# Kernel optimization log

Measured on AMD Instinct MI355X. Metric: run time of the kernel, lower is better.

Reference implementation:

```python
import jax, jax.numpy as jnp
import numpy as np

B, D, RES, NS, MAXS, ITERS = 64, 512, 16, 8, 64, 3
N = RES * RES            # ntokens
HID = max(D, 128)        # mlp hidden = max(dim, hidden_dim)
EPS = 1e-8
BETA = 0.99
SCALE = D ** -0.5


def _grid(res):
    rs = [np.linspace(0.0, 1.0, num=r) for r in (res, res)]
    g = np.stack(np.meshgrid(*rs, sparse=False, indexing='ij'), axis=-1)
    g = g.reshape(res, res, 2)[None].astype(np.float32)
    return jnp.asarray(np.concatenate([g, 1.0 - g], axis=-1))  # (1,res,res,4)


def _ln(x, g, b, axes):
    m = jnp.mean(x, axes, keepdims=True)
    v = jnp.var(x, axes, keepdims=True)
    return (x - m) * jax.lax.rsqrt(v + 1e-5) * g + b


def _gru(x, h, wih, whh, bih, bhh):
    gi = x @ wih.T + bih
    gh = h @ whh.T + bhh
    ir, iz, inn = jnp.split(gi, 3, -1)
    hr, hz, hn = jnp.split(gh, 3, -1)
    r = jax.nn.sigmoid(ir + hr)
    z = jax.nn.sigmoid(iz + hz)
    n = jnp.tanh(inn + r * hn)
    return (1.0 - z) * n + z * h


def setup_inputs() -> dict:
    key = jax.random.key(0)
    ks = iter(jax.random.split(key, 40))
    W = lambda *s: jax.random.normal(next(ks), s, jnp.float32) * 0.02
    Z = lambda *s: jnp.zeros(s, jnp.float32)
    O = lambda *s: jnp.ones(s, jnp.float32)
    inp = dict(
        x=jax.random.normal(next(ks), (B, D, RES, RES), jnp.float32),
        enc_pos_w=W(4, D), enc_pos_b=Z(D),
        enc_norm_g=O(N, D), enc_norm_b=Z(N, D),
        enc_mlp_w1=W(D, D), enc_mlp_b1=Z(D), enc_mlp_w2=W(D, D), enc_mlp_b2=Z(D),
        anch_w1=W(N, N), anch_b1=Z(N), anch_w2=W(N, N), anch_b2=Z(N),
        wq=W(D, D), bq=Z(D), wk=W(D, D), bk=Z(D), wv=W(D, D), bv=Z(D),
        gru_wih=W(3 * D, D), gru_whh=W(3 * D, D), gru_bih=Z(3 * D), gru_bhh=Z(3 * D),
        mlp_w1=W(D, HID), mlp_b1=Z(HID), mlp_w2=W(HID, D), mlp_b2=Z(D),
        ni_g=O(D), ni_b=Z(D), ns_g=O(D), ns_b=Z(D), npf_g=O(D), npf_b=Z(D),
        emb=jax.random.uniform(next(ks), (MAXS, D), jnp.float32, -1.0 / MAXS, 1.0 / MAXS),
        dec_pos_w=W(4, D), dec_pos_b=Z(D),
    )
    return inp


def reference(x, enc_pos_w, enc_pos_b, enc_norm_g, enc_norm_b,
              enc_mlp_w1, enc_mlp_b1, enc_mlp_w2, enc_mlp_b2,
              anch_w1, anch_b1, anch_w2, anch_b2,
              wq, bq, wk, bk, wv, bv,
              gru_wih, gru_whh, gru_bih, gru_bhh,
              mlp_w1, mlp_b1, mlp_w2, mlp_b2,
              ni_g, ni_b, ns_g, ns_b, npf_g, npf_b,
              emb, dec_pos_w, dec_pos_b):
    sg = jax.lax.stop_gradient
    grid = _grid(RES)
    f = jnp.transpose(x, (0, 2, 3, 1))                       # (B,RES,RES,D)
    # encoder_transformation(position=False): flatten + LayerNorm([N,D]) over last 2 dims
    f_np = _ln(f.reshape(B, N, D), enc_norm_g, enc_norm_b, (-2, -1))
    k_nopos = f_np @ wk + bk
    # encoder_transformation(position=True): +pos, LN([N,D]), feature MLP, then norm_input
    pos = grid @ enc_pos_w + enc_pos_b
    fp = _ln((f + pos).reshape(B, N, D), enc_norm_g, enc_norm_b, (-2, -1))
    fp = jax.nn.relu(fp @ enc_mlp_w1 + enc_mlp_b1) @ enc_mlp_w2 + enc_mlp_b2
    fp = _ln(fp, ni_g, ni_b, -1)
    k = fp @ wk + bk
    v = fp @ wv + bv
    # passthrough_eigen_basis on detached k_nopos: normalize, covariance, eigh
    xn = k_nopos / jnp.clip(jnp.linalg.norm(k_nopos, axis=-1, keepdims=True), 1e-12)
    cov = sg(jnp.einsum('bkf,bgf->bkg', xn, xn))             # (B,N,N)
    _, evec = jnp.linalg.eigh(cov)                           # ascending, like symeig
    eig_vec = jnp.transpose(evec[:, :, 1:NS + 1], (0, 2, 1))  # (B,NS,N)
    eig_vec = jax.nn.relu(eig_vec @ anch_w1 + anch_b1) @ anch_w2 + anch_b2
    z = jnp.einsum('bnf,bkn->bkf', f_np, eig_vec)            # masked_projection -> (B,NS,D)
    # sample_slotemb_traditional (euclidean, non-unique, update=0)
    zf = z.reshape(-1, D)
    tslots = emb @ wq + bq                                   # (MAXS,D)
    d2 = (zf ** 2).sum(1, keepdims=True) + (tslots ** 2).sum(1) - 2.0 * zf @ tslots.T
    sampled_dist = d2.min(1)
    idx = jnp.argmin(d2, 1)                                  # (B*NS,)
    # faithful reproduction of the original's index reordering (incl. its cross-batch quirk)
    order = jnp.argsort(sampled_dist.reshape(B, NS), axis=1).reshape(-1)
    idx = idx[order]
    z_q = emb[idx].reshape(B, NS, D)
    t_zq = tslots[idx].reshape(B, NS, D)
    qloss = ((sg(t_zq) - z) ** 2).sum() / B + BETA * ((t_zq - sg(z)) ** 2).sum() / B
    slots = z + sg(z_q - z)                                  # straight-through
    # slot attention iterations
    for _ in range(ITERS):
        slots_prev = slots
        q = _ln(slots, ns_g, ns_b, -1) @ wq + bq
        dots = jnp.einsum('bid,bjd->bij', q, k) * SCALE      # (B,NS,N)
        attn = jax.nn.softmax(dots, axis=1) + EPS            # competition over slots
        attn = attn / attn.sum(-1, keepdims=True)
        updates = jnp.einsum('bjd,bij->bid', v, attn)
        slots = _gru(updates.reshape(-1, D), slots_prev.reshape(-1, D),
                     gru_wih, gru_whh, gru_bih, gru_bhh).reshape(B, NS, D)
        h = _ln(slots, npf_g, npf_b, -1)
        slots = slots + (jax.nn.relu(h @ mlp_w1 + mlp_b1) @ mlp_w2 + mlp_b2)
    # decoder_transformation: broadcast slots over decoder grid + position embed
    dpos = grid @ dec_pos_w + dec_pos_b                      # (1,RES,RES,D)
    df = jnp.broadcast_to(slots.reshape(B * NS, 1, 1, D), (B * NS, RES, RES, D)) + dpos
    feats = jnp.transpose(df, (0, 3, 1, 2))                  # (B*NS,D,RES,RES)
    return feats, slots, idx.reshape(B, NS), qloss
```

## Files before the change

### kernel.cpp

```cpp
#include <hip/hip_runtime.h>
#include <math.h>
#include <stdint.h>


#define NB 64
#define ND 512
#define NN_ 256
#define NSL 8
#define LPB 24

static __device__ __forceinline__ double fsign(double a, double b) {
  return (b >= 0.0) ? fabs(a) : -fabs(a);
}
static __device__ __forceinline__ double dlapy2d(double x, double y) {
  double ax = fabs(x), ay = fabs(y);
  double w = ax > ay ? ax : ay, z = ax > ay ? ay : ax;
  if (z == 0.0) return w;
  double q = z / w;
  return w * sqrt(1.0 + q * q);
}
#define EPS_D 1.1102230246251565e-16

static __device__ void dlartgd(double f, double g, double& cs, double& sn, double& r) {
  if (g == 0.0) { cs = 1.0; sn = 0.0; r = f; }
  else if (f == 0.0) { cs = 0.0; sn = fsign(1.0, g); r = fabs(g); }
  else {
    double f1 = fabs(f);
    double d = sqrt(f * f + g * g);
    cs = f1 / d;
    r = fsign(d, f);
    sn = g / r;
  }
}

static __device__ void dlaev2d(double a, double b, double c, double& rt1, double& rt2,
                               double& cs1, double& sn1) {
  double sm = a + c, df = a - c, adf = fabs(df), tb = b + b, ab = fabs(tb);
  double acmx, acmn;
  if (fabs(a) > fabs(c)) { acmx = a; acmn = c; } else { acmx = c; acmn = a; }
  double rt;
  if (adf > ab) { double q = ab / adf; rt = adf * sqrt(1.0 + q * q); }
  else if (adf < ab) { double q = adf / ab; rt = ab * sqrt(1.0 + q * q); }
  else rt = ab * sqrt(2.0);
  int sgn1;
  if (sm < 0.0) { rt1 = 0.5 * (sm - rt); sgn1 = -1; rt2 = (acmx / rt1) * acmn - (b / rt1) * b; }
  else if (sm > 0.0) { rt1 = 0.5 * (sm + rt); sgn1 = 1; rt2 = (acmx / rt1) * acmn - (b / rt1) * b; }
  else { rt1 = 0.5 * rt; rt2 = -0.5 * rt; sgn1 = 1; }
  double cs; int sgn2;
  if (df >= 0.0) { cs = df + rt; sgn2 = 1; } else { cs = df - rt; sgn2 = -1; }
  double acs = fabs(cs);
  if (acs > ab) { double ct = -tb / cs; sn1 = 1.0 / sqrt(1.0 + ct * ct); cs1 = ct * sn1; }
  else {
    if (ab == 0.0) { cs1 = 1.0; sn1 = 0.0; }
    else { double tn = -cs / tb; cs1 = 1.0 / sqrt(1.0 + tn * tn); sn1 = tn * cs1; }
  }
  if (sgn1 == sgn2) { double tn = cs1; cs1 = -sn1; sn1 = tn; }
}

static __device__ void dsteqr16_lds(double* dd, double* ee, double* zz, int sw) {
  const int n = 16;
#define ZM(i, j) zz[((((i)-1) << 4) + ((j)-1)) ^ sw]
#define D_(i) dd[(i)]
// ... 356 lines not shown
  __syncthreads();
  for (int o = 128; o > 0; o >>= 1) { if (t < o) { s1[t] += s1[t + o]; s2[t] += s2[t + o]; } __syncthreads(); }
  double m = s1[0] / 512.0, var = s2[0] / 512.0 - m * m;
  float rstd = 1.0f / sqrtf((float)var + 1e-5f);
  float mf = (float)m;
  out[(size_t)r * 512 + t] = (v0 - mf) * rstd * g[t] + be[t];
  out[(size_t)r * 512 + t + 256] = (v1 - mf) * rstd * g[t + 256] + be[t + 256];
}

__global__ __launch_bounds__(256) void xnorm_kernel(float* kno) {
  int r = blockIdx.x, t = threadIdx.x;
  __shared__ double s1[256];
  float* row = kno + (size_t)r * 512;
  float v0 = row[t], v1 = row[t + 256];
  s1[t] = (double)v0 * v0 + (double)v1 * v1;
  __syncthreads();
  for (int o = 128; o > 0; o >>= 1) { if (t < o) s1[t] += s1[t + o]; __syncthreads(); }
  float nrm = fmaxf((float)sqrt(s1[0]), 1e-12f);
  row[t] = v0 / nrm; row[t + 256] = v1 / nrm;
}

__global__ __launch_bounds__(256) void cov_kernel(const float* __restrict__ xn, double* __restrict__ cov) {
  int b = blockIdx.x, it = blockIdx.y, jt = blockIdx.z;
  __shared__ float Xi[64][65], Xj[64][65];
  int t = threadIdx.x;
  int tx = t & 15, ty = t >> 4;
  double acc[4][4] = {};
  const float* xb = xn + (size_t)b * 131072;
  for (int f0 = 0; f0 < 512; f0 += 64) {
    for (int l = 0; l < 16; ++l) {
      int idx = t + l * 256;
      int r = idx >> 6, ff = idx & 63;
      Xi[r][ff] = xb[(size_t)(it * 64 + r) * 512 + f0 + ff];
      Xj[r][ff] = xb[(size_t)(jt * 64 + r) * 512 + f0 + ff];
    }
    __syncthreads();
    for (int ff = 0; ff < 64; ++ff) {
      double a0[4], b0[4];
#pragma unroll
      for (int q = 0; q < 4; ++q) { a0[q] = (double)Xi[ty * 4 + q][ff]; b0[q] = (double)Xj[tx * 4 + q][ff]; }
#pragma unroll
      for (int q = 0; q < 4; ++q)
#pragma unroll
        for (int p = 0; p < 4; ++p) acc[q][p] += a0[q] * b0[p];
    }
    __syncthreads();
  }
  double* cb = cov + (size_t)b * 65536;
  for (int q = 0; q < 4; ++q)
    for (int p = 0; p < 4; ++p)
      cb[(size_t)(it * 64 + ty * 4 + q) * 256 + jt * 64 + tx * 4 + p] = acc[q][p];
}

__global__ __launch_bounds__(1024) void dsytrd_kernel(double* Aall, double* dE, double* eE, double* tauE) {
  int b = blockIdx.x, t = threadIdx.x;
  int lane = t & 63, wid = t >> 6;
  double* A = Aall + (size_t)b * 65536;
  __shared__ double v[256], w[256];
  __shared__ double redw[16];
  const int n = 256;
  for (int i = 0; i < n - 1; ++i) {
    double s = 0.0;
    for (int r = i + 2 + t; r < n; r += 1024) { double xv = A[(size_t)r * 256 + i]; s += xv * xv; }
    for (int o = 1; o < 64; o <<= 1) s += __shfl_xor(s, o);
    if (lane == 0) redw[wid] = s;
    __syncthreads();
    double xns = 0.0;
    for (int k = 0; k < 16; ++k) xns += redw[k];
    double alpha = A[(size_t)(i + 1) * 256 + i];
    double tau, beta, scl;
    if (xns == 0.0) { tau = 0.0; beta = alpha; scl = 0.0; }
    else {
      double xnorm = sqrt(xns);
      double rr = dlapy2d(alpha, xnorm);
      beta = (alpha >= 0.0) ? -rr : rr;
      tau = (beta - alpha) / beta;
      scl = 1.0 / (alpha - beta);
    }
    if (tau != 0.0) {
      for (int r = i + 1 + t; r < n; r += 1024) {
        double vr = (r == i + 1) ? 1.0 : A[(size_t)r * 256 + i] * scl;
        v[r] = vr;
        if (r >= i + 2) A[(size_t)r * 256 + i] = vr;
      }
      __syncthreads();
      for (int r = i + 1 + wid; r < n; r += 16) {
        const double* Ar = A + (size_t)r * 256;
        double acc = 0.0;
        for (int c = i + 1 + lane; c < n; c += 64) acc += Ar[c] * v[c];
        for (int o = 1; o < 64; o <<= 1) acc += __shfl_xor(acc, o);
        if (lane == 0) w[r] = tau * acc;
      }
      __syncthreads();
      double sd = 0.0;
      for (int r = i + 1 + t; r < n; r += 1024) sd += w[r] * v[r];
      for (int o = 1; o < 64; o <<= 1) sd += __shfl_xor(sd, o);
      if (lane == 0) redw[wid] = sd;
      __syncthreads();
      double dot = 0.0;
      for (int k = 0; k < 16; ++k) dot += redw[k];
      double alpha2 = -0.5 * tau * dot;
      for (int r = i + 1 + t; r < n; r += 1024) w[r] += alpha2 * v[r];
      __syncthreads();
      for (int r = i + 1 + wid; r < n; r += 16) {
        double vr = v[r], wr = w[r];
        double* Ar = A + (size_t)r * 256;
        for (int c = i + 1 + lane; c < n; c += 64) Ar[c] -= vr * w[c] + wr * v[c];
      }
    }
    if (t == 0) { eE[b * 256 + i] = beta; tauE[b * 256 + i] = tau; }
    __syncthreads();
  }
  for (int r = t; r < n; r += 1024) dE[b * 256 + r] = A[(size_t)r * 256 + r];
}

__global__ __launch_bounds__(64) void tear_kernel(double* dE, const double* eE) {
  int b = threadIdx.x;
  if (b >= 64) return;
  for (int m = 1; m < 16; ++m) {
    int p = m * 16 - 1;
    double ae = fabs(eE[b * 256 + p]);
    dE[b * 256 + p] -= ae;
    dE[b * 256 + p + 1] -= ae;
  }
}

__global__ __launch_bounds__(64) void leaf_kernel(double* dE, double* eE, double* Qe, int* indxq) {
  __shared__ double Zs[LPB * 256];
  __shared__ double des[LPB * 33];
  int t = threadIdx.x;
  int g = blockIdx.x * LPB + t;
  if (t >= LPB || g >= 1024) return;
  int b = g >> 4, lf = g & 15, off = lf * 16;
  double* zz = Zs + t * 256;
  double* dd = des + t * 33;
  double* ee = dd + 16;
  int sw = t & 15;
  for (int i = 1; i <= 16; ++i) dd[i] = dE[b * 256 + off + i - 1];
  for (int i = 1; i <= 15; ++i) ee[i] = eE[b * 256 + off + i - 1];
  ee[16] = 0.0;
  dsteqr16_lds(dd, ee, zz, sw);
  for (int i = 1; i <= 16; ++i) dE[b * 256 + off + i - 1] = dd[i];
  double* Qb = Qe + (size_t)b * 65536;
  for (int r = 0; r < 16; ++r)
    for (int c = 0; c < 16; ++c) Qb[(size_t)(off + r) * 256 + off + c] = zz[((r << 4) + c) ^ sw];
  for (int i = 0; i < 16; ++i) indxq[b * 256 + off + i] = i + 1;
}

__global__ __launch_bounds__(64) void merge_scan_kernel(int nm, int nmerge, double* Qsrc, double* dE,
                                                        const double* eE, int* indxq, double* dlamda_g,
                                                        double* w_g, double* rho_g, int* surv_g,
                                                        int* defl_g, int* Kb) {
  int gid = blockIdx.x * 64 + threadIdx.x;
  if (gid >= 64 * nmerge) return;
  int b = gid / nmerge, mg = gid % nmerge;
  int off = mg * nm, n1 = nm / 2, n2 = nm - n1;
  double* Q = Qsrc + (size_t)b * 65536;
  double* dg = dE + b * 256 + off;
  int* iqg = indxq + b * 256 + off;

  double dl[257], zl[257], dlamA[257], wl2[257];
  int iq[257], indxc[257], indxl[257], indxpl[257];

  for (int i = 1; i <= nm; ++i) { dl[i] = dg[i - 1]; iq[i] = iqg[i - 1]; }
  double rho = eE[b * 256 + off + n1 - 1];
  for (int j = 1; j <= n1; ++j) zl[j] = Q[(size_t)(off + n1 - 1) * 256 + off + j - 1];
  for (int j = 1; j <= n2; ++j) zl[n1 + j] = Q[(size_t)(off + n1) * 256 + off + n1 + j - 1];
  if (rho < 0.0)
    for (int j = n1 + 1; j <= nm; ++j) zl[j] = -zl[j];
  double tconst = 1.0 / sqrt(2.0);
  for (int j = 1; j <= nm; ++j) zl[j] *= tconst;
  rho = fabs(2.0 * rho);
  rho_g[b * nmerge + mg] = rho;
  for (int i = n1 + 1; i <= nm; ++i) iq[i] += n1;
  for (int i = 1; i <= nm; ++i) dlamA[i] = dl[iq[i]];
  dlamrg_dev(n1, n2, dlamA, 1, 1, indxc);
  for (int i = 1; i <= nm; ++i) indxl[i] = iq[indxc[i]];
  int imax = 1, jmax = 1;
  for (int i = 2; i <= nm; ++i) {
    if (fabs(zl[i]) > fabs(zl[imax])) imax = i;
    if (fabs(dl[i]) > fabs(dl[jmax])) jmax = i;
  }
  double tol = 8.0 * EPS_D * fmax(fabs(dl[jmax]), fabs(zl[imax]));
  if (rho * fabs(zl[imax]) <= tol) {
    Kb[b * nmerge + mg] = 0;
    for (int j = 1; j <= nm; ++j) { defl_g[b * 256 + off + j - 1] = indxl[j]; dlamA[j] = dl[indxl[j]]; }
    for (int j = 1; j <= nm; ++j) { dg[j - 1] = dlamA[j]; iqg[j - 1] = j; }
    return;
  }
  int K = 0, K2 = nm + 1, pj = 0, j = 1;
  bool havepj = false;
  for (j = 1; j <= nm; ++j) {
    int nj = indxl[j];
    if (rho * fabs(zl[nj]) <= tol) {
      K2--; indxpl[K2] = nj;
      if (j == nm) break;
    } else { pj = nj; havepj = true; break; }
  }
  if (havepj) {
    for (;;) {
      j = j + 1;
      if (j > nm) break;
      int nj = indxl[j];
      if (rho * fabs(zl[nj]) <= tol) { K2--; indxpl[K2] = nj; }
      else {
        double s_ = zl[pj], c_ = zl[nj];
        double tau_ = dlapy2d(c_, s_);
        double t_ = dl[nj] - dl[pj];
        c_ = c_ / tau_; s_ = -s_ / tau_;
        if (fabs(t_ * c_ * s_) <= tol) {
          zl[nj] = tau_; zl[pj] = 0.0;
          int cp = off + pj - 1, cn = off + nj - 1;
          for (int r = 0; r < nm; ++r) {
            size_t rowb = (size_t)(off + r) * 256;
            double x = Q[rowb + cp], y = Q[rowb + cn];
            Q[rowb + cp] = c_ * x + s_ * y;
            Q[rowb + cn] = c_ * y - s_ * x;
          }
          double t2 = dl[pj] * c_ * c_ + dl[nj] * s_ * s_;
          dl[nj] = dl[pj] * s_ * s_ + dl[nj] * c_ * c_;
          dl[pj] = t2;
          K2--;
          int i_ = 1;
          for (;;) {
            if (K2 + i_ <= nm) {
              if (dl[pj] < dl[indxpl[K2 + i_]]) {
                indxpl[K2 + i_ - 1] = indxpl[K2 + i_];
                indxpl[K2 + i_] = pj;
                i_++;
              } else { indxpl[K2 + i_ - 1] = pj; break; }
            } else { indxpl[K2 + i_ - 1] = pj; break; }
          }
          pj = nj;
        } else {
          K++; dlamA[K] = dl[pj]; wl2[K] = zl[pj]; indxpl[K] = pj; pj = nj;
        }
      }
    }
    K++; dlamA[K] = dl[pj]; wl2[K] = zl[pj]; indxpl[K] = pj;
  }
  Kb[b * nmerge + mg] = K;
  for (int i = 1; i <= K; ++i) {
    dlamda_g[b * 256 + off + i - 1] = dlamA[i];
    w_g[b * 256 + off + i - 1] = wl2[i];
    surv_g[b * 256 + off + i - 1] = indxpl[i];
  }
  for (int jj = K + 1; jj <= nm; ++jj) {
    defl_g[b * 256 + off + jj - 1] = indxpl[jj];
    dg[jj - 1] = dl[indxpl[jj]];
  }
}

__global__ __launch_bounds__(256) void secular_kernel(int nm, int nmerge, const double* dlamda_g,
                                                      const double* w_g, const double* rho_g,
                                                      const int* Kb, double* dE, double* tau_g,
                                                      int* orig_g) {
  int b = blockIdx.x, pos = threadIdx.x;
  int mg = pos / nm, jl = pos % nm + 1;
  int K = Kb[b * nmerge + mg];
  if (jl > K) return;
  int base = b * 256 + mg * nm;
  const double* dl = dlamda_g + base;
  const double* w = w_g + base;
  double rho = rho_g[b * nmerge + mg];
  int orig; double lo, hi;
  if (jl < K) {
    double dj = dl[jl - 1], dj1 = dl[jl];
    double mid = (dj + dj1) * 0.5;
    double acc = 0.0;
    for (int i = 0; i < K; ++i) acc += w[i] * w[i] / (dl[i] - mid);
    double fmid = 1.0 + rho * acc;
    if (fmid > 0.0) { orig = jl; lo = 0.0; hi = mid - dj; }
    else { orig = jl + 1; lo = mid - dj1; hi = 0.0; }
  } else {
    orig = K;
    double zs = 0.0;
    for (int i = 0; i < K; ++i) zs += w[i] * w[i];
    lo = 0.0; hi = rho * zs;
  }
  double dorig = dl[orig - 1];
  for (int it = 0; it < 100; ++it) {
    double tm = 0.5 * (lo + hi);
    if (tm == lo || tm == hi) break;
    double acc = 0.0;
    for (int i = 0; i < K; ++i) acc += w[i] * w[i] / ((dl[i] - dorig) - tm);
    double g = 1.0 + rho * acc;
    if (g > 0.0) hi = tm; else lo = tm;
  }
  double tau = 0.5 * (lo + hi);
  tau_g[base + jl - 1] = tau;
  orig_g[base + jl - 1] = orig;
  dE[base + jl - 1] = dorig + tau;
}

__global__ __launch_bounds__(256) void zhat_kernel(int nm, int nmerge, const double* dlamda_g,
                                                   const double* w_g, const double* tau_g,
                                                   const int* orig_g, const int* Kb, double* zhat_g) {
  int b = blockIdx.x, pos = threadIdx.x;
  int mg = pos / nm, il = pos % nm + 1;
  int K = Kb[b * nmerge + mg];
  if (il > K) return;
  int base = b * 256 + mg * nm;
// ... 51 lines not shown
    if (dg[ind1 - 1] <= dg[ind2 - 1]) { idx[i++] = ind1; ind1++; n1sv--; }
    else { idx[i++] = ind2; ind2--; n2sv--; }
  }
  if (n1sv == 0) { while (n2sv > 0) { idx[i++] = ind2; ind2--; n2sv--; } }
  else { while (n1sv > 0) { idx[i++] = ind1; ind1++; n1sv--; } }
  for (int t = 1; t <= nm; ++t) iqg[t - 1] = idx[t];
}

__global__ __launch_bounds__(256) void merge_gemm_kernel(int nm, int nmerge, const double* Qsrc,
                                                         const double* Cbuf, const int* surv_g,
                                                         const int* Kb, double* Qdst) {
  int b = blockIdx.x, mg = blockIdx.y;
  int tcnt = nm / 32;
  int rt = blockIdx.z / tcnt, ct = blockIdx.z % tcnt;
  int off = mg * nm;
  int K = Kb[b * nmerge + mg];
  if (ct * 32 >= K) return;
  __shared__ double Qs[32][33];
  __shared__ double Cs[32][33];
  __shared__ int svs[32];
  int t = threadIdx.x;
  int tc = t & 31, tr = t >> 5;
  const double* Qsb = Qsrc + (size_t)b * 65536;
  const double* Cb = Cbuf + (size_t)b * 65536;
  double acc[4] = {0, 0, 0, 0};
  int r0 = off + rt * 32, c0 = off + ct * 32;
  for (int i0 = 0; i0 < K; i0 += 32) {
    if (t < 32) svs[t] = (i0 + t < K) ? surv_g[b * 256 + off + i0 + t] : 0;
    __syncthreads();
    for (int l = 0; l < 4; ++l) {
      int idx = t + l * 256;
      int r = idx >> 5, ii = idx & 31;
      int sc = svs[ii];
      Qs[r][ii] = (sc > 0) ? Qsb[(size_t)(r0 + r) * 256 + off + sc - 1] : 0.0;
      Cs[r][ii] = (i0 + r < K && ct * 32 + ii < K) ? Cb[(size_t)(off + i0 + r) * 256 + c0 + ii] : 0.0;
    }
    __syncthreads();
    for (int ii = 0; ii < 32; ++ii) {
      double cv = Cs[ii][tc];
#pragma unroll
      for (int q = 0; q < 4; ++q) acc[q] += Qs[tr * 4 + q][ii] * cv;
    }
    __syncthreads();
  }
  if (ct * 32 + tc < K) {
    double* Qd = Qdst + (size_t)b * 65536;
    for (int q = 0; q < 4; ++q) Qd[(size_t)(r0 + tr * 4 + q) * 256 + c0 + tc] = acc[q];
  }
}

__global__ __launch_bounds__(256) void defl_copy_kernel(int nm, int nmerge, const double* Qsrc,
                                                        const int* defl_g, const int* Kb,
                                                        double* Qdst) {
  int b = blockIdx.x, pos = threadIdx.x;
  int mg = pos / nm, jl = pos % nm + 1;
  int K = Kb[b * nmerge + mg];
  if (jl <= K) return;
  int off = mg * nm;
  int srcc = off + defl_g[b * 256 + off + jl - 1] - 1;
  int dstc = off + jl - 1;
  const double* Qs = Qsrc + (size_t)b * 65536;
  double* Qd = Qdst + (size_t)b * 65536;
  for (int r = 0; r < nm; ++r) Qd[(size_t)(off + r) * 256 + dstc] = Qs[(size_t)(off + r) * 256 + srcc];
}

__global__ __launch_bounds__(256) void dormtr_kernel(const double* Aall, const double* tauE,
                                                     const double* Qe, const int* indxq, float* E) {
  int b = blockIdx.x, t = threadIdx.x;
  const double* A = Aall + (size_t)b * 65536;
  __shared__ double U[256][8];
  __shared__ double wred[32][8];
  __shared__ double wfin[8];
  __shared__ int sel[8];
  if (t < 8) sel[t] = indxq[b * 256 + 1 + t] - 1;
  __syncthreads();
  for (int i = t; i < 256 * 8; i += 256) {
    int r = i >> 3, c = i & 7;
    U[r][c] = Qe[(size_t)b * 65536 + (size_t)r * 256 + sel[c]];
  }
  __syncthreads();
  int lane = t & 31, col = t >> 5;
  for (int s = 254; s >= 0; --s) {
    double tv = tauE[b * 256 + s];
    if (tv == 0.0) continue;
    double acc = (lane == 0) ? U[s + 1][col] : 0.0;
    for (int r = s + 2 + lane; r < 256; r += 32) acc += A[(size_t)r * 256 + s] * U[r][col];
    wred[lane][col] = acc;
    __syncthreads();
    if (t < 8) { double a = 0.0; for (int l2 = 0; l2 < 32; ++l2) a += wred[l2][t]; wfin[t] = a; }
    __syncthreads();
    double wc = wfin[col] * tv;
    if (lane == 0) U[s + 1][col] -= wc;
    for (int r = s + 2 + lane; r < 256; r += 32) U[r][col] -= A[(size_t)r * 256 + s] * wc;
    __syncthreads();
  }
  for (int i = t; i < 8 * 256; i += 256) {
    int s = i >> 8, nn = i & 255;
    E[((size_t)b * 8 + s) * 256 + nn] = (float)U[nn][s];
  }
}

__global__ __launch_bounds__(256) void zproj_kernel(const float* __restrict__ fnp,
                                                    const float* __restrict__ E2,
                                                    float* __restrict__ z) {
  int b = blockIdx.x, s = blockIdx.y;
  __shared__ float er[256];
  int t = threadIdx.x;
  er[t] = E2[((size_t)b * 8 + s) * 256 + t];
  __syncthreads();
  for (int d = t; d < 512; d += 256) {
    float acc = 0.f;
    for (int n = 0; n < 256; ++n) acc += er[n] * fnp[((size_t)b * 256 + n) * 512 + d];
    z[((size_t)b * 8 + s) * 512 + d] = acc;
  }
}

__global__ __launch_bounds__(64) void d2_kernel(const float* __restrict__ z,
                                                const float* __restrict__ ts, double* sdist,
                                                int* idxr) {
  int row = blockIdx.x;
  int lane = threadIdx.x;
  const float* zr = z + (size_t)row * 512;
  const float* tr = ts + (size_t)lane * 512;
  double zz = 0, zt = 0, tt = 0;
  for (int d = 0; d < 512; ++d) {
    double zv = zr[d], tv = tr[d];
    zz += zv * zv; zt += zv * tv; tt += tv * tv;
  }
  double d2 = zz + tt - 2.0 * zt;
  int best = lane; double bv = d2;
  for (int off = 32; off > 0; off >>= 1) {
    double ov = __shfl_down(bv, off);
    int oi = __shfl_down(best, off);
    if (ov < bv || (ov == bv && oi < best)) { bv = ov; best = oi; }
  }
  if (lane == 0) { sdist[row] = bv; idxr[row] = best; }
}

__global__ __launch_bounds__(64) void order_kernel(const double* sdist, const int* idxr, int* fidx,
                                                   float* out_idx) {
  int b = threadIdx.x;
  if (b >= 64) return;
  double sd[8]; int ord[8];
  for (int s = 0; s < 8; ++s) { sd[s] = sdist[b * 8 + s]; ord[s] = s; }
  for (int a = 1; a < 8; ++a) {
    double kv = sd[a]; int ko = ord[a]; int c = a - 1;
    while (c >= 0 && sd[c] > kv) { sd[c + 1] = sd[c]; ord[c + 1] = ord[c]; --c; }
    sd[c + 1] = kv; ord[c + 1] = ko;
  }
  for (int s = 0; s < 8; ++s) {
    int fi = idxr[ord[s]];
    fidx[b * 8 + s] = fi;
    out_idx[b * 8 + s] = (float)fi;
  }
}

__global__ __launch_bounds__(256) void slots0_kernel(const float* z, const float* emb,
                                                     const int* fidx, float* slots) {
  int i = blockIdx.x * 256 + threadIdx.x;
  if (i >= 512 * 512) return;
  int t = i / 512, d = i % 512;
  float zv = z[i];
  float zq = emb[fidx[t] * 512 + d];
  slots[i] = zv + (zq - zv);
}

// ... 183 lines not shown
  int* defl_g = (int*)alloc(64 * 256 * 4);
  int* orig_g = (int*)alloc(64 * 256 * 4);
  int* Kb = (int*)alloc(64 * 8 * 4);
  int* fidx = (int*)alloc(512 * 4);
  float* E = (float*)alloc(64 * 8 * 256 * 4);
  float* Eh = (float*)alloc(64 * 8 * 256 * 4);
  float* E2 = (float*)alloc(64 * 8 * 256 * 4);
  float* z = (float*)alloc(512 * 512 * 4);
  float* tslots = (float*)alloc(64 * 512 * 4);
  double* sdist = (double*)alloc(512 * 8);
  int* idxr = (int*)alloc(512 * 4);
  float* sA = (float*)alloc(512 * 512 * 4);
  float* sB = (float*)alloc(512 * 512 * 4);
  float* lnbuf = (float*)alloc(512 * 512 * 4);
  float* qbuf = (float*)alloc(512 * 512 * 4);
  float* dotsb = (float*)alloc(64 * 8 * 256 * 4);
  float* attnb = (float*)alloc(64 * 8 * 256 * 4);
  float* asumb = (float*)alloc(64 * 8 * 4);
  float* updb = (float*)alloc(512 * 512 * 4);
  float* gib = (float*)alloc((size_t)512 * 1536 * 4);
  float* ghb = (float*)alloc((size_t)512 * 1536 * 4);
  float* hidb = (float*)alloc(512 * 512 * 4);
  (void)ws_size; (void)in_sizes; (void)n_in; (void)out_size;

  auto gemm = [&](const float* A, const float* Bm, const float* bias, const float* base, float* C,
                  int M, int Nc, int Kd, int bt, int act, int addb) {
    if ((M % 128) == 0 && (Nc % 128) == 0 && (Kd % 16) == 0) {
      dim3 g(M / 128, Nc / 128);
      gemm_f32_big<<<g, 256, 0, stream>>>(A, Bm, bias, base, C, M, Nc, Kd, bt, act, addb);
    } else {
      dim3 g((M + 63) / 64, (Nc + 63) / 64);
      gemm_f32<<<g, 256, 0, stream>>>(A, Bm, bias, base, C, M, Nc, Kd, bt, act, addb);
    }
  };

  pos_kernel<<<(131072 + 255) / 256, 256, 0, stream>>>(enc_pos_w, enc_pos_b, posT);
  pos_kernel<<<(131072 + 255) / 256, 256, 0, stream>>>(dec_pos_w, dec_pos_b, dposT);
  stats_kernel<<<64, 256, 0, stream>>>(x, posT, m1, r1, 0);
  stats_kernel<<<64, 256, 0, stream>>>(x, posT, m2, r2, 1);
  tln_kernel<<<dim3(64, 16, 8), 256, 0, stream>>>(x, posT, enc_norm_g, enc_norm_b, m1, r1, m2, r2,
                                                  fnp, R3);
  gemm(fnp, wk, bk, nullptr, R2, 16384, 512, 512, 0, 0, 0);
  gemm(R3, enc_mlp_w1, enc_mlp_b1, nullptr, R4, 16384, 512, 512, 0, 1, 0);
  gemm(R4, enc_mlp_w2, enc_mlp_b2, nullptr, R5, 16384, 512, 512, 0, 0, 0);
  rowln_kernel<<<16384, 256, 0, stream>>>(R5, ni_g, ni_b, R5);
  gemm(R5, wk, bk, nullptr, kbuf, 16384, 512, 512, 0, 0, 0);
  gemm(R5, wv, bv, nullptr, vbuf, 16384, 512, 512, 0, 0, 0);
  xnorm_kernel<<<16384, 256, 0, stream>>>(R2);
  double* covA = (double*)R3;
  cov_kernel<<<dim3(64, 4, 4), 256, 0, stream>>>(R2, covA);
  double* Qe = (double*)R4;
  double* Q2 = (double*)R5;
  double* Cbuf = (double*)R2;
  hipMemsetAsync(Qe, 0, S, stream);
  hipMemsetAsync(Q2, 0, S, stream);
  dsytrd_kernel<<<64, 1024, 0, stream>>>(covA, dE, eE, tauE);
  tear_kernel<<<1, 64, 0, stream>>>(dE, eE);
  leaf_kernel<<<(1024 + LPB - 1) / LPB, LPB, 0, stream>>>(dE, eE, Qe, indxq);
  for (int L = 0; L < 4; ++L) {
    int nm = 32 << L;
    int nmerge = 256 / nm;
    double* src = (L % 2 == 0) ? Qe : Q2;
    double* dst = (L % 2 == 0) ? Q2 : Qe;
    int gScan = (64 * nmerge + 63) / 64;
    merge_scan_kernel<<<gScan, 64, 0, stream>>>(nm, nmerge, src, dE, eE, indxq, dlamda_g, w_g, rho_g,
                                                surv_g, defl_g, Kb);
    secular_kernel<<<64, 256, 0, stream>>>(nm, nmerge, dlamda_g, w_g, rho_g, Kb, dE, tau_g, orig_g);
    zhat_kernel<<<64, 256, 0, stream>>>(nm, nmerge, dlamda_g, w_g, tau_g, orig_g, Kb, zhat_g);
    coeff_kernel<<<64, 256, 0, stream>>>(nm, nmerge, dlamda_g, zhat_g, tau_g, orig_g, Kb, Cbuf);
    int tcnt = nm / 32;
    merge_gemm_kernel<<<dim3(64, nmerge, tcnt * tcnt), 256, 0, stream>>>(nm, nmerge, src, Cbuf,
                                                                         surv_g, Kb, dst);
    defl_copy_kernel<<<64, 256, 0, stream>>>(nm, nmerge, src, defl_g, Kb, dst);
    dlamrg_kernel<<<gScan, 64, 0, stream>>>(nm, nmerge, dE, Kb, indxq);
  }
  dormtr_kernel<<<64, 256, 0, stream>>>(covA, tauE, Qe, indxq, E);
  gemm(E, anch_w1, anch_b1, nullptr, Eh, 512, 256, 256, 0, 1, 0);
  gemm(Eh, anch_w2, anch_b2, nullptr, E2, 512, 256, 256, 0, 0, 0);
  zproj_kernel<<<dim3(64, 8), 256, 0, stream>>>(fnp, E2, z);
  gemm(emb, wq, bq, nullptr, tslots, 64, 512, 512, 0, 0, 0);
  d2_kernel<<<512, 64, 0, stream>>>(z, tslots, sdist, idxr);
  order_kernel<<<1, 64, 0, stream>>>(sdist, idxr, fidx, out_idx);
  slots0_kernel<<<1024, 256, 0, stream>>>(z, emb, fidx, sA);
  qloss_kernel<<<1, 256, 0, stream>>>(z, tslots, fidx, out_qloss);
  for (int it = 0; it < 3; ++it) {
    rowln_kernel<<<512, 256, 0, stream>>>(sA, ns_g, ns_b, lnbuf);
    gemm(lnbuf, wq, bq, nullptr, qbuf, 512, 512, 512, 0, 0, 0);
    dots_kernel<<<dim3(64, 4), 256, 0, stream>>>(qbuf, kbuf, dotsb);
    softmax_kernel<<<64, 256, 0, stream>>>(dotsb, attnb);
    asum_kernel<<<512, 64, 0, stream>>>(attnb, asumb);
    updates_kernel<<<64, 256, 0, stream>>>(attnb, asumb, vbuf, updb);
    gemm(updb, gru_wih, gru_bih, nullptr, gib, 512, 1536, 512, 1, 0, 0);
    gemm(sA, gru_whh, gru_bhh, nullptr, ghb, 512, 1536, 512, 1, 0, 0);
    gru_kernel<<<1024, 256, 0, stream>>>(gib, ghb, sA, sB);
    rowln_kernel<<<512, 256, 0, stream>>>(sB, npf_g, npf_b, lnbuf);
    gemm(lnbuf, mlp_w1, mlp_b1, nullptr, hidb, 512, 512, 512, 0, 1, 0);
    gemm(hidb, mlp_w2, mlp_b2, sB, sA, 512, 512, 512, 0, 0, 1);
  }
  feats_kernel<<<262144, 64, 0, stream>>>(sA, dposT, out);
  hipMemcpyAsync(out_slots, sA, 262144 * 4, hipMemcpyDeviceToDevice, stream);
}
```

Measured before the change: 16.44 ms.

## Block dsytrd with panel updates, parallelize merge scan, defl copy and zproj

```diff
diff --git a/kernel.cpp b/kernel.cpp
--- a/kernel.cpp
+++ b/kernel.cpp
@@ -8,6 +8,8 @@
 #define NN_ 256
 #define NSL 8
 #define LPB 24
+#define TNB 32
+#define VWROWS 260
 
 static __device__ __forceinline__ double fsign(double a, double b) {
   return (b >= 0.0) ? fabs(a) : -fabs(a);
@@ -470,64 +472,132 @@
       cb[(size_t)(it * 64 + ty * 4 + q) * 256 + jt * 64 + tx * 4 + p] = acc[q][p];
 }
 
-__global__ __launch_bounds__(1024) void dsytrd_kernel(double* Aall, double* dE, double* eE, double* tauE) {
+__global__ __launch_bounds__(1024) void dsytrd_kernel(double* Aall, double* dE, double* eE,
+                                                      double* tauE, double* Vw, double* Ww) {
   int b = blockIdx.x, t = threadIdx.x;
   int lane = t & 63, wid = t >> 6;
   double* A = Aall + (size_t)b * 65536;
+  double* V = Vw + (size_t)b * (VWROWS * TNB);
+  double* W = Ww + (size_t)b * (VWROWS * TNB);
   __shared__ double v[256], w[256];
   __shared__ double redw[16];
+  __shared__ double wvv[TNB], vvv[TNB];
   const int n = 256;
-  for (int i = 0; i < n - 1; ++i) {
-    double s = 0.0;
-    for (int r = i + 2 + t; r < n; r += 1024) { double xv = A[(size_t)r * 256 + i]; s += xv * xv; }
-    for (int o = 1; o < 64; o <<= 1) s += __shfl_xor(s, o);
-    if (lane == 0) redw[wid] = s;
-    __syncthreads();
-    double xns = 0.0;
-    for (int k = 0; k < 16; ++k) xns += redw[k];
-    double alpha = A[(size_t)(i + 1) * 256 + i];
-    double tau, beta, scl;
-    if (xns == 0.0) { tau = 0.0; beta = alpha; scl = 0.0; }
-    else {
-      double xnorm = sqrt(xns);
-      double rr = dlapy2d(alpha, xnorm);
-      beta = (alpha >= 0.0) ? -rr : rr;
-      tau = (beta - alpha) / beta;
-      scl = 1.0 / (alpha - beta);
-    }
-    if (tau != 0.0) {
-      for (int r = i + 1 + t; r < n; r += 1024) {
-        double vr = (r == i + 1) ? 1.0 : A[(size_t)r * 256 + i] * scl;
-        v[r] = vr;
-        if (r >= i + 2) A[(size_t)r * 256 + i] = vr;
+  for (int i0 = 0; i0 < n - 1; i0 += TNB) {
+    int jend = (TNB < (n - 1) - i0) ? TNB : (n - 1) - i0;
+    for (int j = 0; j < jend; ++j) {
+      int i = i0 + j;
+      if (j > 0) {
+        for (int r = i + t; r < n; r += 1024) {
+          double acc = A[(size_t)r * 256 + i];
+          const double* Vr = V + (size_t)r * TNB;
+          const double* Wr = W + (size_t)r * TNB;
+          const double* Vi = V + (size_t)i * TNB;
+          const double* Wi = W + (size_t)i * TNB;
+          for (int q = 0; q < j; ++q) acc -= Vr[q] * Wi[q] + Wr[q] * Vi[q];
+          A[(size_t)r * 256 + i] = acc;
+        }
+        __syncthreads();
+      }
+      double s = 0.0;
+      for (int r = i + 2 + t; r < n; r += 1024) { double xv = A[(size_t)r * 256 + i]; s += xv * xv; }
+      for (int o = 1; o < 64; o <<= 1) s += __shfl_xor(s, o);
+      if (lane == 0) redw[wid] = s;
+      __syncthreads();
+      double xns = 0.0;
+      for (int k = 0; k < 16; ++k) xns += redw[k];
+      double alpha = A[(size_t)(i + 1) * 256 + i];
+      double tau, beta, scl;
+      if (xns == 0.0) { tau = 0.0; beta = alpha; scl = 0.0; }
+      else {
+        double xnorm = sqrt(xns);
+        double rr = dlapy2d(alpha, xnorm);
+        beta = (alpha >= 0.0) ? -rr : rr;
+        tau = (beta - alpha) / beta;
+        scl = 1.0 / (alpha - beta);
+      }
+      if (tau != 0.0) {
+        for (int r = i0 + 1 + t; r < n; r += 1024) {
+          double vr;
+          if (r < i + 1) vr = 0.0;
+          else if (r == i + 1) vr = 1.0;
+          else vr = A[(size_t)r * 256 + i] * scl;
+          if (r >= i + 1) v[r] = vr;
+          if (r >= i + 2) A[(size_t)r * 256 + i] = vr;
+          V[(size_t)r * TNB + j] = vr;
+        }
+        __syncthreads();
+        if (j > 0) {
+          for (int q = wid; q < j; q += 16) {
+            double aw = 0.0, av = 0.0;
+            for (int r = i + 1 + lane; r < n; r += 64) {
+              double vr = v[r];
+              aw += W[(size_t)r * TNB + q] * vr;
+              av += V[(size_t)r * TNB + q] * vr;
+            }
+            for (int o = 1; o < 64; o <<= 1) { aw += __shfl_xor(aw, o); av += __shfl_xor(av, o); }
+            if (lane == 0) { wvv[q] = aw; vvv[q] = av; }
+          }
+          __syncthreads();
+        }
+        for (int r = i + 1 + wid; r < n; r += 16) {
+          const double* Ar = A + (size_t)r * 256;
+          double acc = 0.0;
+          for (int c = i + 1 + lane; c < n; c += 64) acc += Ar[c] * v[c];
+          if (lane < j)
+            acc -= V[(size_t)r * TNB + lane] * wvv[lane] + W[(size_t)r * TNB + lane] * vvv[lane];
+          for (int o = 1; o < 64; o <<= 1) acc += __shfl_xor(acc, o);
+          if (lane == 0) w[r] = tau * acc;
+        }
+        __syncthreads();
+        double sd = 0.0;
+        for (int r = i + 1 + t; r < n; r += 1024) sd += w[r] * v[r];
+        for (int o = 1; o < 64; o <<= 1) sd += __shfl_xor(sd, o);
+        if (lane == 0) redw[wid] = sd;
+        __syncthreads();
+        double dot = 0.0;
+        for (int k = 0; k < 16; ++k) dot += redw[k];
+        double alpha2 = -0.5 * tau * dot;
+        for (int r = i0 + 1 + t; r < n; r += 1024) {
+          double wr = (r >= i + 1) ? (w[r] + alpha2 * v[r]) : 0.0;
+          if (r >= i + 1) w[r] = wr;
+          W[(size_t)r * TNB + j] = wr;
+        }
+        __syncthreads();
+      } else {
+        for (int r = i0 + 1 + t; r < n; r += 1024) {
+          V[(size_t)r * TNB + j] = 0.0;
+          W[(size_t)r * TNB + j] = 0.0;
+        }
+        __syncthreads();
+      }
+      if (t == 0) { eE[b * 256 + i] = beta; tauE[b * 256 + i] = tau; }
+      __syncthreads();
+    }
+    int rs = i0 + jend;
+    if (rs < n) {
+      for (int r0 = rs + wid * 4; r0 < n; r0 += 64) {
+        for (int c = rs + lane; c < n; c += 64) {
+          double a0 = 0.0, a1 = 0.0, a2 = 0.0, a3 = 0.0;
+          const double* Vc = V + (size_t)c * TNB;
+          const double* Wc = W + (size_t)c * TNB;
+          const double* Vr = V + (size_t)r0 * TNB;
+          const double* Wr = W + (size_t)r0 * TNB;
+          for (int q = 0; q < jend; ++q) {
+            double vc = Vc[q], wc = Wc[q];
+            a0 += Vr[q] * wc + Wr[q] * vc;
+            a1 += Vr[TNB + q] * wc + Wr[TNB + q] * vc;
+            a2 += Vr[2 * TNB + q] * wc + Wr[2 * TNB + q] * vc;
+            a3 += Vr[3 * TNB + q] * wc + Wr[3 * TNB + q] * vc;
+          }
+          A[(size_t)r0 * 256 + c] -= a0;
+          if (r0 + 1 < n) A[(size_t)(r0 + 1) * 256 + c] -= a1;
+          if (r0 + 2 < n) A[(size_t)(r0 + 2) * 256 + c] -= a2;
+          if (r0 + 3 < n) A[(size_t)(r0 + 3) * 256 + c] -= a3;
+        }
       }
       __syncthreads();
-      for (int r = i + 1 + wid; r < n; r += 16) {
-        const double* Ar = A + (size_t)r * 256;
-        double acc = 0.0;
-        for (int c = i + 1 + lane; c < n; c += 64) acc += Ar[c] * v[c];
-        for (int o = 1; o < 64; o <<= 1) acc += __shfl_xor(acc, o);
-        if (lane == 0) w[r] = tau * acc;
-      }
-      __syncthreads();
-      double sd = 0.0;
-      for (int r = i + 1 + t; r < n; r += 1024) sd += w[r] * v[r];
-      for (int o = 1; o < 64; o <<= 1) sd += __shfl_xor(sd, o);
-      if (lane == 0) redw[wid] = sd;
-      __syncthreads();
-      double dot = 0.0;
-      for (int k = 0; k < 16; ++k) dot += redw[k];
-      double alpha2 = -0.5 * tau * dot;
-      for (int r = i + 1 + t; r < n; r += 1024) w[r] += alpha2 * v[r];
-      __syncthreads();
-      for (int r = i + 1 + wid; r < n; r += 16) {
-        double vr = v[r], wr = w[r];
-        double* Ar = A + (size_t)r * 256;
-        for (int c = i + 1 + lane; c < n; c += 64) Ar[c] -= vr * w[c] + wr * v[c];
-      }
-    }
-    if (t == 0) { eE[b * 256 + i] = beta; tauE[b * 256 + i] = tau; }
-    __syncthreads();
+    }
   }
   for (int r = t; r < n; r += 1024) dE[b * 256 + r] = A[(size_t)r * 256 + r];
 }
@@ -565,107 +635,130 @@
   for (int i = 0; i < 16; ++i) indxq[b * 256 + off + i] = i + 1;
 }
 
-__global__ __launch_bounds__(64) void merge_scan_kernel(int nm, int nmerge, double* Qsrc, double* dE,
-                                                        const double* eE, int* indxq, double* dlamda_g,
-                                                        double* w_g, double* rho_g, int* surv_g,
-                                                        int* defl_g, int* Kb) {
-  int gid = blockIdx.x * 64 + threadIdx.x;
-  if (gid >= 64 * nmerge) return;
-  int b = gid / nmerge, mg = gid % nmerge;
+__global__ __launch_bounds__(256) void merge_scan_kernel(int nm, int nmerge, double* Qsrc, double* dE,
+                                                         const double* eE, int* indxq,
+                                                         double* dlamda_g, double* w_g, double* rho_g,
+                                                         int* surv_g, int* defl_g, int* Kb) {
+  int b = blockIdx.x, mg = blockIdx.y;
   int off = mg * nm, n1 = nm / 2, n2 = nm - n1;
   double* Q = Qsrc + (size_t)b * 65536;
   double* dg = dE + b * 256 + off;
   int* iqg = indxq + b * 256 + off;
-
-  double dl[257], zl[257], dlamA[257], wl2[257];
-  int iq[257], indxc[257], indxl[257], indxpl[257];
-
-  for (int i = 1; i <= nm; ++i) { dl[i] = dg[i - 1]; iq[i] = iqg[i - 1]; }
-  double rho = eE[b * 256 + off + n1 - 1];
-  for (int j = 1; j <= n1; ++j) zl[j] = Q[(size_t)(off + n1 - 1) * 256 + off + j - 1];
-  for (int j = 1; j <= n2; ++j) zl[n1 + j] = Q[(size_t)(off + n1) * 256 + off + n1 + j - 1];
-  if (rho < 0.0)
-    for (int j = n1 + 1; j <= nm; ++j) zl[j] = -zl[j];
-  double tconst = 1.0 / sqrt(2.0);
-  for (int j = 1; j <= nm; ++j) zl[j] *= tconst;
-  rho = fabs(2.0 * rho);
-  rho_g[b * nmerge + mg] = rho;
-  for (int i = n1 + 1; i <= nm; ++i) iq[i] += n1;
-  for (int i = 1; i <= nm; ++i) dlamA[i] = dl[iq[i]];
-  dlamrg_dev(n1, n2, dlamA, 1, 1, indxc);
-  for (int i = 1; i <= nm; ++i) indxl[i] = iq[indxc[i]];
-  int imax = 1, jmax = 1;
-  for (int i = 2; i <= nm; ++i) {
-    if (fabs(zl[i]) > fabs(zl[imax])) imax = i;
-    if (fabs(dl[i]) > fabs(dl[jmax])) jmax = i;
-  }
-  double tol = 8.0 * EPS_D * fmax(fabs(dl[jmax]), fabs(zl[imax]));
-  if (rho * fabs(zl[imax]) <= tol) {
-    Kb[b * nmerge + mg] = 0;
-    for (int j = 1; j <= nm; ++j) { defl_g[b * 256 + off + j - 1] = indxl[j]; dlamA[j] = dl[indxl[j]]; }
-    for (int j = 1; j <= nm; ++j) { dg[j - 1] = dlamA[j]; iqg[j - 1] = j; }
-    return;
-  }
-  int K = 0, K2 = nm + 1, pj = 0, j = 1;
-  bool havepj = false;
-  for (j = 1; j <= nm; ++j) {
-    int nj = indxl[j];
-    if (rho * fabs(zl[nj]) <= tol) {
-      K2--; indxpl[K2] = nj;
-      if (j == nm) break;
-    } else { pj = nj; havepj = true; break; }
-  }
-  if (havepj) {
-    for (;;) {
-      j = j + 1;
-      if (j > nm) break;
-      int nj = indxl[j];
-      if (rho * fabs(zl[nj]) <= tol) { K2--; indxpl[K2] = nj; }
-      else {
-        double s_ = zl[pj], c_ = zl[nj];
-        double tau_ = dlapy2d(c_, s_);
-        double t_ = dl[nj] - dl[pj];
-        c_ = c_ / tau_; s_ = -s_ / tau_;
-        if (fabs(t_ * c_ * s_) <= tol) {
-          zl[nj] = tau_; zl[pj] = 0.0;
-          int cp = off + pj - 1, cn = off + nj - 1;
-          for (int r = 0; r < nm; ++r) {
-            size_t rowb = (size_t)(off + r) * 256;
-            double x = Q[rowb + cp], y = Q[rowb + cn];
-            Q[rowb + cp] = c_ * x + s_ * y;
-            Q[rowb + cn] = c_ * y - s_ * x;
+  int t = threadIdx.x;
+
+  __shared__ double dl[257], zl[257], dlamA[257], wl2[257];
+  __shared__ int iq[257], indxc[257], indxl[257], indxpl[257];
+  __shared__ double rotc[256], rots[256];
+  __shared__ int rotp[256], rotn[256];
+  __shared__ int sh_nrot, sh_K, sh_zero;
+
+  for (int ii = 1 + t; ii <= nm; ii += 256) { dl[ii] = dg[ii - 1]; iq[ii] = iqg[ii - 1]; }
+  __syncthreads();
+
+  if (t == 0) {
+    double rho = eE[b * 256 + off + n1 - 1];
+    for (int j = 1; j <= n1; ++j) zl[j] = Q[(size_t)(off + n1 - 1) * 256 + off + j - 1];
+    for (int j = 1; j <= n2; ++j) zl[n1 + j] = Q[(size_t)(off + n1) * 256 + off + n1 + j - 1];
+    if (rho < 0.0)
+      for (int j = n1 + 1; j <= nm; ++j) zl[j] = -zl[j];
+    double tconst = 1.0 / sqrt(2.0);
+    for (int j = 1; j <= nm; ++j) zl[j] *= tconst;
+    rho = fabs(2.0 * rho);
+    rho_g[b * nmerge + mg] = rho;
+    for (int i = n1 + 1; i <= nm; ++i) iq[i] += n1;
+    for (int i = 1; i <= nm; ++i) dlamA[i] = dl[iq[i]];
+    dlamrg_dev(n1, n2, dlamA, 1, 1, indxc);
+    for (int i = 1; i <= nm; ++i) indxl[i] = iq[indxc[i]];
+    int imax = 1, jmax = 1;
+    for (int i = 2; i <= nm; ++i) {
+      if (fabs(zl[i]) > fabs(zl[imax])) imax = i;
+      if (fabs(dl[i]) > fabs(dl[jmax])) jmax = i;
+    }
+    double tol = 8.0 * EPS_D * fmax(fabs(dl[jmax]), fabs(zl[imax]));
+    if (rho * fabs(zl[imax]) <= tol) {
+      sh_K = 0; sh_zero = 1; sh_nrot = 0;
+    } else {
+      sh_zero = 0;
+      int nrot = 0;
+      int K = 0, K2 = nm + 1, pj = 0, j = 1;
+      bool havepj = false;
+      for (j = 1; j <= nm; ++j) {
+        int nj = indxl[j];
+        if (rho * fabs(zl[nj]) <= tol) {
+          K2--; indxpl[K2] = nj;
+          if (j == nm) break;
+        } else { pj = nj; havepj = true; break; }
+      }
+      if (havepj) {
+        for (;;) {
+          j = j + 1;
+          if (j > nm) break;
+          int nj = indxl[j];
+          if (rho * fabs(zl[nj]) <= tol) { K2--; indxpl[K2] = nj; }
+          else {
+            double s_ = zl[pj], c_ = zl[nj];
+            double tau_ = dlapy2d(c_, s_);
+            double t_ = dl[nj] - dl[pj];
+            c_ = c_ / tau_; s_ = -s_ / tau_;
+            if (fabs(t_ * c_ * s_) <= tol) {
+              zl[nj] = tau_; zl[pj] = 0.0;
+              rotp[nrot] = pj; rotn[nrot] = nj; rotc[nrot] = c_; rots[nrot] = s_; ++nrot;
+              double t2 = dl[pj] * c_ * c_ + dl[nj] * s_ * s_;
+              dl[nj] = dl[pj] * s_ * s_ + dl[nj] * c_ * c_;
+              dl[pj] = t2;
+              K2--;
+              int i_ = 1;
+              for (;;) {
+                if (K2 + i_ <= nm) {
+                  if (dl[pj] < dl[indxpl[K2 + i_]]) {
+                    indxpl[K2 + i_ - 1] = indxpl[K2 + i_];
+                    indxpl[K2 + i_] = pj;
+                    i_++;
+                  } else { indxpl[K2 + i_ - 1] = pj; break; }
+                } else { indxpl[K2 + i_ - 1] = pj; break; }
+              }
+              pj = nj;
+            } else {
+              K++; dlamA[K] = dl[pj]; wl2[K] = zl[pj]; indxpl[K] = pj; pj = nj;
+            }
           }
-          double t2 = dl[pj] * c_ * c_ + dl[nj] * s_ * s_;
-          dl[nj] = dl[pj] * s_ * s_ + dl[nj] * c_ * c_;
-          dl[pj] = t2;
-          K2--;
-          int i_ = 1;
-          for (;;) {
-            if (K2 + i_ <= nm) {
-              if (dl[pj] < dl[indxpl[K2 + i_]]) {
-                indxpl[K2 + i_ - 1] = indxpl[K2 + i_];
-                indxpl[K2 + i_] = pj;
-                i_++;
-              } else { indxpl[K2 + i_ - 1] = pj; break; }
-            } else { indxpl[K2 + i_ - 1] = pj; break; }
-          }
-          pj = nj;
-        } else {
-          K++; dlamA[K] = dl[pj]; wl2[K] = zl[pj]; indxpl[K] = pj; pj = nj;
         }
+        K++; dlamA[K] = dl[pj]; wl2[K] = zl[pj]; indxpl[K] = pj;
       }
-    }
-    K++; dlamA[K] = dl[pj]; wl2[K] = zl[pj]; indxpl[K] = pj;
-  }
-  Kb[b * nmerge + mg] = K;
-  for (int i = 1; i <= K; ++i) {
-    dlamda_g[b * 256 + off + i - 1] = dlamA[i];
-    w_g[b * 256 + off + i - 1] = wl2[i];
-    surv_g[b * 256 + off + i - 1] = indxpl[i];
-  }
-  for (int jj = K + 1; jj <= nm; ++jj) {
-    defl_g[b * 256 + off + jj - 1] = indxpl[jj];
-    dg[jj - 1] = dl[indxpl[jj]];
+      sh_K = K; sh_nrot = nrot;
+    }
+  }
+  __syncthreads();
+  int nrot = sh_nrot, K = sh_K;
+  for (int r = t; r < nm; r += 256) {
+    size_t rowb = (size_t)(off + r) * 256;
+    for (int k = 0; k < nrot; ++k) {
+      int cp = off + rotp[k] - 1, cn = off + rotn[k] - 1;
+      double c_ = rotc[k], s_ = rots[k];
+      double x = Q[rowb + cp], y = Q[rowb + cn];
+      Q[rowb + cp] = c_ * x + s_ * y;
+      Q[rowb + cn] = c_ * y - s_ * x;
+    }
+  }
+  if (sh_zero) {
+    if (t == 0) Kb[b * nmerge + mg] = 0;
+    for (int j = 1 + t; j <= nm; j += 256) {
+      int il = indxl[j];
+      defl_g[b * 256 + off + j - 1] = il;
+      dg[j - 1] = dl[il];
+      iqg[j - 1] = j;
+    }
+  } else {
+    if (t == 0) Kb[b * nmerge + mg] = K;
+    for (int i = 1 + t; i <= K; i += 256) {
+      dlamda_g[b * 256 + off + i - 1] = dlamA[i];
+      w_g[b * 256 + off + i - 1] = wl2[i];
+      surv_g[b * 256 + off + i - 1] = indxpl[i];
+    }
+    for (int jj = K + 1 + t; jj <= nm; jj += 256) {
+      defl_g[b * 256 + off + jj - 1] = indxpl[jj];
+      dg[jj - 1] = dl[indxpl[jj]];
+    }
   }
 }
 
@@ -823,16 +916,18 @@
 __global__ __launch_bounds__(256) void defl_copy_kernel(int nm, int nmerge, const double* Qsrc,
                                                         const int* defl_g, const int* Kb,
                                                         double* Qdst) {
-  int b = blockIdx.x, pos = threadIdx.x;
-  int mg = pos / nm, jl = pos % nm + 1;
+  int b = blockIdx.x, mg = blockIdx.y;
+  int off = mg * nm;
   int K = Kb[b * nmerge + mg];
-  if (jl <= K) return;
-  int off = mg * nm;
-  int srcc = off + defl_g[b * 256 + off + jl - 1] - 1;
-  int dstc = off + jl - 1;
+  int t = threadIdx.x;
   const double* Qs = Qsrc + (size_t)b * 65536;
   double* Qd = Qdst + (size_t)b * 65536;
-  for (int r = 0; r < nm; ++r) Qd[(size_t)(off + r) * 256 + dstc] = Qs[(size_t)(off + r) * 256 + srcc];
+  for (int r = t; r < nm; r += 256) {
+    const double* Qsr = Qs + (size_t)(off + r) * 256;
+    double* Qdr = Qd + (size_t)(off + r) * 256;
+    for (int jl = K + 1; jl <= nm; ++jl)
+      Qdr[off + jl - 1] = Qsr[off + defl_g[b * 256 + off + jl - 1] - 1];
+  }
 }
 
 __global__ __launch_bounds__(256) void dormtr_kernel(const double* Aall, const double* tauE,
@@ -874,15 +969,26 @@
 __global__ __launch_bounds__(256) void zproj_kernel(const float* __restrict__ fnp,
                                                     const float* __restrict__ E2,
                                                     float* __restrict__ z) {
-  int b = blockIdx.x, s = blockIdx.y;
-  __shared__ float er[256];
-  int t = threadIdx.x;
-  er[t] = E2[((size_t)b * 8 + s) * 256 + t];
+  int b = blockIdx.x, t = threadIdx.x;
+  __shared__ float er[8][256];
+  for (int i = t; i < 8 * 256; i += 256) er[i >> 8][i & 255] = E2[(size_t)b * 2048 + i];
   __syncthreads();
-  for (int d = t; d < 512; d += 256) {
-    float acc = 0.f;
-    for (int n = 0; n < 256; ++n) acc += er[n] * fnp[((size_t)b * 256 + n) * 512 + d];
-    z[((size_t)b * 8 + s) * 512 + d] = acc;
+  for (int d0 = 0; d0 < 512; d0 += 256) {
+    int d = d0 + t;
+    float a0 = 0.f, a1 = 0.f, a2 = 0.f, a3 = 0.f, a4 = 0.f, a5 = 0.f, a6 = 0.f, a7 = 0.f;
+    for (int n = 0; n < 256; ++n) {
+      float f = fnp[((size_t)b * 256 + n) * 512 + d];
+      a0 += er[0][n] * f; a1 += er[1][n] * f; a2 += er[2][n] * f; a3 += er[3][n] * f;
+      a4 += er[4][n] * f; a5 += er[5][n] * f; a6 += er[6][n] * f; a7 += er[7][n] * f;
+    }
+    z[((size_t)b * 8 + 0) * 512 + d] = a0;
+    z[((size_t)b * 8 + 1) * 512 + d] = a1;
+    z[((size_t)b * 8 + 2) * 512 + d] = a2;
+    z[((size_t)b * 8 + 3) * 512 + d] = a3;
+    z[((size_t)b * 8 + 4) * 512 + d] = a4;
+    z[((size_t)b * 8 + 5) * 512 + d] = a5;
+    z[((size_t)b * 8 + 6) * 512 + d] = a6;
+    z[((size_t)b * 8 + 7) * 512 + d] = a7;
   }
 }
 
@@ -1172,9 +1278,11 @@
   double* Qe = (double*)R4;
   double* Q2 = (double*)R5;
   double* Cbuf = (double*)R2;
+  double* Vw = (double*)R2;
+  double* Ww = Vw + (size_t)64 * VWROWS * TNB;
   hipMemsetAsync(Qe, 0, S, stream);
   hipMemsetAsync(Q2, 0, S, stream);
-  dsytrd_kernel<<<64, 1024, 0, stream>>>(covA, dE, eE, tauE);
+  dsytrd_kernel<<<64, 1024, 0, stream>>>(covA, dE, eE, tauE, Vw, Ww);
   tear_kernel<<<1, 64, 0, stream>>>(dE, eE);
   leaf_kernel<<<(1024 + LPB - 1) / LPB, LPB, 0, stream>>>(dE, eE, Qe, indxq);
   for (int L = 0; L < 4; ++L) {
@@ -1183,21 +1291,21 @@
     double* src = (L % 2 == 0) ? Qe : Q2;
     double* dst = (L % 2 == 0) ? Q2 : Qe;
     int gScan = (64 * nmerge + 63) / 64;
-    merge_scan_kernel<<<gScan, 64, 0, stream>>>(nm, nmerge, src, dE, eE, indxq, dlamda_g, w_g, rho_g,
-                                                surv_g, defl_g, Kb);
+    merge_scan_kernel<<<dim3(64, nmerge), 256, 0, stream>>>(nm, nmerge, src, dE, eE, indxq,
+                                                            dlamda_g, w_g, rho_g, surv_g, defl_g, Kb);
     secular_kernel<<<64, 256, 0, stream>>>(nm, nmerge, dlamda_g, w_g, rho_g, Kb, dE, tau_g, orig_g);
     zhat_kernel<<<64, 256, 0, stream>>>(nm, nmerge, dlamda_g, w_g, tau_g, orig_g, Kb, zhat_g);
     coeff_kernel<<<64, 256, 0, stream>>>(nm, nmerge, dlamda_g, zhat_g, tau_g, orig_g, Kb, Cbuf);
     int tcnt = nm / 32;
     merge_gemm_kernel<<<dim3(64, nmerge, tcnt * tcnt), 256, 0, stream>>>(nm, nmerge, src, Cbuf,
                                                                          surv_g, Kb, dst);
-    defl_copy_kernel<<<64, 256, 0, stream>>>(nm, nmerge, src, defl_g, Kb, dst);
+    defl_copy_kernel<<<dim3(64, nmerge), 256, 0, stream>>>(nm, nmerge, src, defl_g, Kb, dst);
     dlamrg_kernel<<<gScan, 64, 0, stream>>>(nm, nmerge, dE, Kb, indxq);
   }
   dormtr_kernel<<<64, 256, 0, stream>>>(covA, tauE, Qe, indxq, E);
   gemm(E, anch_w1, anch_b1, nullptr, Eh, 512, 256, 256, 0, 1, 0);
   gemm(Eh, anch_w2, anch_b2, nullptr, E2, 512, 256, 256, 0, 0, 0);
-  zproj_kernel<<<dim3(64, 8), 256, 0, stream>>>(fnp, E2, z);
+  zproj_kernel<<<64, 256, 0, stream>>>(fnp, E2, z);
   gemm(emb, wq, bq, nullptr, tslots, 64, 512, 512, 0, 0, 0);
   d2_kernel<<<512, 64, 0, stream>>>(z, tslots, sdist, idxr);
   order_kernel<<<1, 64, 0, stream>>>(sdist, idxr, fidx, out_idx);
```

After: 18.07 ms. +9.9%, slower.
